# Optimization experiments

Hardware: AMD Instinct MI355X
Metric: run time of the kernel (lower is better)

The kernel has to match this reference:

```python
import jax, jax.numpy as jnp
import numpy as np

DIM = 768
HEADS = 12
HEAD_DIM = DIM // HEADS
HIDDEN = int(DIM * 4.0)
EPS = 1e-5


def _layernorm(x, g, b):
    mu = jnp.mean(x, axis=-1, keepdims=True)
    var = jnp.mean(jnp.square(x - mu), axis=-1, keepdims=True)
    return (x - mu) * jax.lax.rsqrt(var + EPS) * g + b


def setup_inputs() -> dict:
    key = jax.random.key(0)
    ks = jax.random.split(key, 8)
    s_in = 1.0 / np.sqrt(DIM)
    s_hid = 1.0 / np.sqrt(HIDDEN)
    return {
        "x": jax.random.normal(ks[0], (2, 2048, DIM), dtype=jnp.float32),
        "ln1_g": jnp.ones((DIM,), jnp.float32),
        "ln1_b": jnp.zeros((DIM,), jnp.float32),
        "w_qkv": jax.random.normal(ks[1], (DIM, 3 * DIM), jnp.float32) * s_in,
        "w_proj": jax.random.normal(ks[2], (DIM, DIM), jnp.float32) * s_in,
        "b_proj": jnp.zeros((DIM,), jnp.float32),
        "ln2_g": jnp.ones((DIM,), jnp.float32),
        "ln2_b": jnp.zeros((DIM,), jnp.float32),
        "w_fc1": jax.random.normal(ks[3], (DIM, HIDDEN), jnp.float32) * s_in,
        "b_fc1": jnp.zeros((HIDDEN,), jnp.float32),
        "w_fc2": jax.random.normal(ks[4], (HIDDEN, DIM), jnp.float32) * s_hid,
        "b_fc2": jnp.zeros((DIM,), jnp.float32),
    }


def reference(x, ln1_g, ln1_b, w_qkv, w_proj, b_proj, ln2_g, ln2_b, w_fc1, b_fc1, w_fc2, b_fc2):
    b, n, c = x.shape
    scale = HEAD_DIM ** -0.5

    # --- attention branch ---
    h = _layernorm(x, ln1_g, ln1_b)
    qkv = (h @ w_qkv).reshape(b, n, 3, HEADS, HEAD_DIM)
    q, k, v = jnp.moveaxis(qkv, 2, 0)          # each [b, n, H, hd]
    attn = jnp.einsum("bqhd,bkhd->bhqk", q, k) * scale
    attn = jax.nn.softmax(attn, axis=-1)       # [b, H, n, n] (naive, materialized)
    o = jnp.einsum("bhqk,bkhd->bqhd", attn, v).reshape(b, n, c)
    x = x + o @ w_proj + b_proj

    # --- MLP branch ---
    h2 = _layernorm(x, ln2_g, ln2_b)
    m = jax.nn.gelu(h2 @ w_fc1 + b_fc1, approximate=False)
    x = x + m @ w_fc2 + b_fc2
    return x
```

## Files before the change

kernel.cpp:

```cpp
#include <hip/hip_runtime.h>
#include <math.h>


typedef unsigned short u16;
typedef __attribute__((ext_vector_type(8))) short short8;
typedef __attribute__((ext_vector_type(4))) float f32x4;

#define TOKENS 4096
#define DIM    768
#define QKV_N  2304
#define HID    3072
#define NSEQ   2048
#define NHEAD  12
#define HDIM   64

__device__ __forceinline__ float bf2f(u16 u) {
  union { unsigned i; float f; } v; v.i = ((unsigned)u) << 16; return v.f;
}
__device__ __forceinline__ u16 f2bf(float f) {
  union { float f; unsigned i; } v; v.f = f;
  unsigned r = v.i + 0x7fffu + ((v.i >> 16) & 1u);
  return (u16)(r >> 16);
}
__device__ __forceinline__ unsigned cvt_pk_bf16(float lo, float hi) {
  unsigned r;
  asm("v_cvt_pk_bf16_f32 %0, %1, %2" : "=v"(r) : "v"(lo), "v"(hi));
  return r;
}
__device__ __forceinline__ void pl32swap(unsigned &a, unsigned &b) {
  asm("v_permlane32_swap_b32 %0, %1" : "+v"(a), "+v"(b));
}
__device__ __forceinline__ void pl16swap(unsigned &a, unsigned &b) {
  asm("v_permlane16_swap_b32 %0, %1" : "+v"(a), "+v"(b));
}

__device__ __forceinline__ void async_copy16(const u16* g, u16* l) {
  __builtin_amdgcn_global_load_lds(
      (const __attribute__((address_space(1))) unsigned int*)(unsigned long long)g,
      (__attribute__((address_space(3))) unsigned int*)(unsigned int)(unsigned long long)l,
      16, 0, 0);
}

__global__ __launch_bounds__(256) void prep_kernel(
    const float* __restrict__ x, const float* __restrict__ g,
    const float* __restrict__ b, u16* __restrict__ h,
    const float* __restrict__ in0, u16* __restrict__ out0,
    const float* __restrict__ in1, u16* __restrict__ out1,
    const float* __restrict__ in2, u16* __restrict__ out2,
    const float* __restrict__ in3, u16* __restrict__ out3) {
  const int tid = threadIdx.x;
  if (blockIdx.x < 1024) {
    int wave = tid >> 6, lane = tid & 63;
    int token = blockIdx.x * 4 + wave;
    float v[12];
    const float4* xr = (const float4*)(x + (size_t)token * DIM);
#pragma unroll
    for (int w = 0; w < 3; w++) {
      float4 q = xr[lane + w * 64];
      v[w * 4 + 0] = q.x; v[w * 4 + 1] = q.y; v[w * 4 + 2] = q.z; v[w * 4 + 3] = q.w;
    }
    float s = 0.f;
#pragma unroll
    for (int i = 0; i < 12; i++) s += v[i];
#pragma unroll
    for (int off = 32; off > 0; off >>= 1) s += __shfl_xor(s, off);
    float mu = s * (1.0f / DIM);
    float ss = 0.f;
#pragma unroll
    for (int i = 0; i < 12; i++) { float d = v[i] - mu; ss += d * d; }
#pragma unroll
    for (int off = 32; off > 0; off >>= 1) ss += __shfl_xor(ss, off);
    float rs = rsqrtf(ss * (1.0f / DIM) + 1e-5f);
    ushort4* orow = (ushort4*)(h + (size_t)token * DIM);
    const float4* g4 = (const float4*)g;
    const float4* b4 = (const float4*)b;
#pragma unroll
    for (int w = 0; w < 3; w++) {
      float4 gq = g4[lane + w * 64], bq = b4[lane + w * 64];
      ushort4 o;
      o.x = f2bf((v[w * 4 + 0] - mu) * rs * gq.x + bq.x);
      o.y = f2bf((v[w * 4 + 1] - mu) * rs * gq.y + bq.y);
      o.z = f2bf((v[w * 4 + 2] - mu) * rs * gq.z + bq.z);
      o.w = f2bf((v[w * 4 + 3] - mu) * rs * gq.w + bq.w);
      orow[lane + w * 64] = o;
    }
    return;
  }
  __shared__ u16 t[32][33];
  int bid = blockIdx.x - 1024, rem;
  const float* in; u16* out; int R, C;
  if (bid < 1728)      { in = in0; out = out0; R = 768;  C = 2304; rem = bid; }
  else if (bid < 2304) { in = in1; out = out1; R = 768;  C = 768;  rem = bid - 1728; }
  else if (bid < 4608) { in = in2; out = out2; R = 768;  C = 3072; rem = bid - 2304; }
  else                 { in = in3; out = out3; R = 3072; C = 768;  rem = bid - 4608; }
  int c0 = (rem % (C / 32)) * 32, r0 = (rem / (C / 32)) * 32;
  int tx = tid & 31, ty = tid >> 5;
#pragma unroll
  for (int i = 0; i < 4; i++)
    t[ty + i * 8][tx] = f2bf(in[(size_t)(r0 + ty + i * 8) * C + c0 + tx]);
  __syncthreads();
#pragma unroll
  for (int i = 0; i < 4; i++)
    out[(size_t)(c0 + ty + i * 8) * R + r0 + tx] = t[tx][ty + i * 8];
}

__global__ __launch_bounds__(256) void ln_kernel(const u16* __restrict__ xin,
                                                 const float* __restrict__ g,
                                                 const float* __restrict__ b,
                                                 u16* __restrict__ out) {
  int wave = threadIdx.x >> 6, lane = threadIdx.x & 63;
  int token = blockIdx.x * 4 + wave;
  float v[12];
  const ushort4* xr = (const ushort4*)(xin + (size_t)token * DIM);
#pragma unroll
  for (int w = 0; w < 3; w++) {
    ushort4 q = xr[lane + w * 64];
    v[w * 4 + 0] = bf2f(q.x); v[w * 4 + 1] = bf2f(q.y);
    v[w * 4 + 2] = bf2f(q.z); v[w * 4 + 3] = bf2f(q.w);
  }
  float s = 0.f;
#pragma unroll
  for (int i = 0; i < 12; i++) s += v[i];
#pragma unroll
  for (int off = 32; off > 0; off >>= 1) s += __shfl_xor(s, off);
  float mu = s * (1.0f / DIM);
  float ss = 0.f;
#pragma unroll
  for (int i = 0; i < 12; i++) { float d = v[i] - mu; ss += d * d; }
#pragma unroll
  for (int off = 32; off > 0; off >>= 1) ss += __shfl_xor(ss, off);
  float rs = rsqrtf(ss * (1.0f / DIM) + 1e-5f);

  ushort4* orow = (ushort4*)(out + (size_t)token * DIM);
  const float4* g4 = (const float4*)g;
  const float4* b4 = (const float4*)b;
#pragma unroll
  for (int w = 0; w < 3; w++) {
    float4 gq = g4[lane + w * 64], bq = b4[lane + w * 64];
    ushort4 o;
    o.x = f2bf((v[w * 4 + 0] - mu) * rs * gq.x + bq.x);
    o.y = f2bf((v[w * 4 + 1] - mu) * rs * gq.y + bq.y);
    o.z = f2bf((v[w * 4 + 2] - mu) * rs * gq.z + bq.z);
    o.w = f2bf((v[w * 4 + 3] - mu) * rs * gq.w + bq.w);
    orow[lane + w * 64] = o;
  }
}

template <int BM, int BN, int EPI, int NP>
__global__ __launch_bounds__(256, 3) void gemm_bt(
    const u16* __restrict__ A, const u16* __restrict__ BT,
    void* __restrict__ Cout, const float* __restrict__ bias,
    const void* __restrict__ resid, int M, int N, int K,
    u16* __restrict__ vtb) {
  constexpr int MT = BM / 32, NT = BN / 32;
  constexpr int ACH = BM / 16;
  constexpr int CPW = (BM + BN) / 64;
  __shared__ __align__(16) u16 Alds[NP][BM * 32];
  __shared__ __align__(16) u16 Blds[NP][BN * 32];
  const int tid = threadIdx.x;
  const int lane = tid & 63, wave = tid >> 6;
  const int wr = wave >> 1, wc = wave & 1;
  const int nby = M / BM;
  const int by = blockIdx.x % nby, bx = blockIdx.x / nby;
  const int bm = by * BM, bn = bx * BN;
  const int c16 = lane & 15, quad = lane >> 4;
  const int l4 = lane >> 2;
  const int lc = (((lane & 3) ^ ((l4 >> 1) & 3)) * 8);
  const int fsw = (c16 >> 1) & 3;

  f32x4 acc[MT][NT];
#pragma unroll
  for (int i = 0; i < MT; i++)
#pragma unroll
    for (int j = 0; j < NT; j++) acc[i][j] = (f32x4){0.f, 0.f, 0.f, 0.f};

  const u16* gsrc[CPW];
  u16* ldst[CPW];
  int hstep[CPW];
#pragma unroll
  for (int c = 0; c < CPW; c++) {
    int chunk = wave * CPW + c;
    if (chunk < ACH) {
      gsrc[c] = A + (size_t)(bm + chunk * 16 + l4) * K + lc;
      ldst[c] = Alds[0] + chunk * 512;
      hstep[c] = BM * 32;
    } else {
      int bc = chunk - ACH;
      gsrc[c] = BT + (size_t)(bn + bc * 16 + l4) * K + lc;
      ldst[c] = Blds[0] + bc * 512;
      hstep[c] = BN * 32;
    }
  }

  for (int kk = 0; kk < K; kk += 32 * NP) {
    __syncthreads();
#pragma unroll
    for (int c = 0; c < CPW; c++)
#pragma unroll
      for (int p = 0; p < NP; p++)
        async_copy16(gsrc[c] + kk + 32 * p, ldst[c] + p * hstep[c]);
    __syncthreads();
#pragma unroll
    for (int ks = 0; ks < NP; ks++) {
      short8 af[MT], bfr[NT];
#pragma unroll
      for (int mt = 0; mt < MT; mt++)
        af[mt] = *(const short8*)(Alds[ks] + (wr * (BM / 2) + mt * 16 + c16) * 32 +
                                  ((quad ^ fsw)) * 8);
#pragma unroll
      for (int nt = 0; nt < NT; nt++)
        bfr[nt] = *(const short8*)(Blds[ks] + (wc * (BN / 2) + nt * 16 + c16) * 32 +
                                   ((quad ^ fsw)) * 8);
#pragma unroll
      for (int mt = 0; mt < MT; mt++)
#pragma unroll
        for (int nt = 0; nt < NT; nt++)
          acc[mt][nt] = __builtin_amdgcn_mfma_f32_16x16x32_bf16(af[mt], bfr[nt],
                                                                acc[mt][nt], 0, 0, 0);
    }
  }

#pragma unroll
  for (int mt = 0; mt < MT; mt++) {
#pragma unroll
    for (int nt = 0; nt < NT; nt++) {
      int col = bn + wc * (BN / 2) + nt * 16 + c16;
      float bv = (EPI != 0) ? bias[col] : 0.f;
      int row0 = bm + wr * (BM / 2) + mt * 16 + quad * 4;
      if (EPI == 0 && col >= 2 * DIM) {
        int b = row0 >> 11;
        ushort4 pk;
        pk.x = f2bf(acc[mt][nt][0]); pk.y = f2bf(acc[mt][nt][1]);
        pk.z = f2bf(acc[mt][nt][2]); pk.w = f2bf(acc[mt][nt][3]);
        *(ushort4*)(vtb + ((size_t)b * DIM + col - 2 * DIM) * NSEQ + (row0 & 2047)) = pk;
        continue;
      }
#pragma unroll
      for (int r = 0; r < 4; r++) {
        int row = row0 + r;
        float vv = acc[mt][nt][r];
        if (EPI == 1) {
          vv += bv + ((const float*)resid)[(size_t)row * N + col];
          ((u16*)Cout)[(size_t)row * N + col] = f2bf(vv);
        } else if (EPI == 2) {
          vv += bv;
          vv = 0.5f * vv * (1.0f + erff(vv * 0.70710678118654752f));
          ((u16*)Cout)[(size_t)row * N + col] = f2bf(vv);
        } else if (EPI == 3) {
          vv += bv + bf2f(((const u16*)resid)[(size_t)row * N + col]);
          ((float*)Cout)[(size_t)row * N + col] = vv;
        } else {
          ((u16*)Cout)[(size_t)row * N + col] = f2bf(vv);
        }
      }
    }
  }
}

__global__ __launch_bounds__(256, 3) void attn_kernel(const u16* __restrict__ qkv,
                                                      const u16* __restrict__ vt,
                                                      u16* __restrict__ o) {
  const int tid = threadIdx.x;
  const int lane = tid & 63, wave = tid >> 6;
  const int c16 = lane & 15, quad = lane >> 4;
  const int wq = wave >> 1, wk = wave & 1;
  const int bh = blockIdx.x % (2 * NHEAD);
  const int qt = blockIdx.x / (2 * NHEAD);
  const int bb = bh / NHEAD, h = bh % NHEAD;
  __shared__ __align__(16) u16 Klds[2][64 * 64];
  __shared__ __align__(16) u16 Vtlds[2][64 * 64];
  const size_t base = (size_t)bb * NSEQ * QKV_N;
  const int q0 = qt * 64;
  const int sw = c16 & 7;

  short8 qf[2][2];
#pragma unroll
  for (int qs = 0; qs < 2; qs++) {
    const u16* qp = qkv + base + (size_t)(q0 + wq * 32 + qs * 16 + c16) * QKV_N + h * HDIM;
    qf[qs][0] = *(const short8*)(qp + quad * 8);
    qf[qs][1] = *(const short8*)(qp + 32 + quad * 8);
  }

  float Ls[2] = {0.f, 0.f};
  f32x4 Of[2][4];
#pragma unroll
  for (int qs = 0; qs < 2; qs++)
#pragma unroll
    for (int dt = 0; dt < 4; dt++) Of[qs][dt] = (f32x4){0.f, 0.f, 0.f, 0.f};

  const int srow = lane >> 3;
  const int schunk = (lane & 7) ^ srow;
  const int r0 = wave * 16;
  const u16* ksrc = qkv + base + (size_t)(r0 + srow) * QKV_N + DIM + h * HDIM + schunk * 8;
  const u16* vsrc = vt + ((size_t)bh * HDIM + r0 + srow) * NSEQ + schunk * 8;
  const float SC = 0.18033688011112042f;

#pragma unroll
  for (int j = 0; j < 2; j++) {
    async_copy16(ksrc + (size_t)(8 * j) * QKV_N, Klds[0] + r0 * 64 + 8 * j * 64);
    async_copy16(vsrc + (size_t)(8 * j) * NSEQ, Vtlds[0] + r0 * 64 + 8 * j * 64);
  }

  for (int it = 0; it < NSEQ / 64; it++) {
    const int cur = it & 1;
    __syncthreads();
    if (it + 1 < NSEQ / 64) {
      const int kt1 = (it + 1) * 64;
      u16* kd = Klds[cur ^ 1] + r0 * 64;
      u16* vd = Vtlds[cur ^ 1] + r0 * 64;
#pragma unroll
      for (int j = 0; j < 2; j++) {
        async_copy16(ksrc + (size_t)(kt1 + 8 * j) * QKV_N, kd + 8 * j * 64);
        async_copy16(vsrc + (size_t)(8 * j) * NSEQ + kt1, vd + 8 * j * 64);
      }
    }

    short8 kf0[2], kf1[2];
#pragma unroll
    for (int kt = 0; kt < 2; kt++) {
      const u16* krow = Klds[cur] + (wk * 32 + kt * 16 + c16) * 64;
      kf0[kt] = *(const short8*)(krow + (quad ^ sw) * 8);
      kf1[kt] = *(const short8*)(krow + ((quad + 4) ^ sw) * 8);
    }

    f32x4 St[2][2];
#pragma unroll
    for (int qs = 0; qs < 2; qs++)
#pragma unroll
      for (int kt = 0; kt < 2; kt++) {
        f32x4 s = (f32x4){0.f, 0.f, 0.f, 0.f};
        s = __builtin_amdgcn_mfma_f32_16x16x32_bf16(kf0[kt], qf[qs][0], s, 0, 0, 0);
        s = __builtin_amdgcn_mfma_f32_16x16x32_bf16(kf1[kt], qf[qs][1], s, 0, 0, 0);
        St[qs][kt] = s;
      }

    short8 vf[4];
#pragma unroll
    for (int dt = 0; dt < 4; dt++) {
      const u16* vrow = Vtlds[cur] + (dt * 16 + c16) * 64;
      vf[dt] = *(const short8*)(vrow + ((wk * 4 + quad) ^ sw) * 8);
    }

    short8 pf[2];
#pragma unroll
    for (int qs = 0; qs < 2; qs++) {
      float p[2][4];
#pragma unroll
      for (int kt = 0; kt < 2; kt++)
#pragma unroll
        for (int r = 0; r < 4; r++)
          p[kt][r] = __builtin_amdgcn_exp2f(St[qs][kt][r] * SC);
      Ls[qs] += ((p[0][0] + p[0][1]) + (p[0][2] + p[0][3])) +
                ((p[1][0] + p[1][1]) + (p[1][2] + p[1][3]));
      unsigned a0 = cvt_pk_bf16(p[0][0], p[0][1]);
      unsigned a1 = cvt_pk_bf16(p[0][2], p[0][3]);
      unsigned b0 = cvt_pk_bf16(p[1][0], p[1][1]);
      unsigned b1 = cvt_pk_bf16(p[1][2], p[1][3]);
      pl32swap(a0, b0);
      pl32swap(a1, b1);
      pl16swap(a0, b0);
      pl16swap(a1, b1);
      union { unsigned u[4]; short8 s; } pk_;
      pk_.u[0] = a0; pk_.u[1] = a1; pk_.u[2] = b0; pk_.u[3] = b1;
      pf[qs] = pk_.s;
    }

#pragma unroll
    for (int dt = 0; dt < 4; dt++)
#pragma unroll
      for (int qs = 0; qs < 2; qs++)
        Of[qs][dt] = __builtin_amdgcn_mfma_f32_16x16x32_bf16(pf[qs], vf[dt],
                                                             Of[qs][dt], 0, 0, 0);
  }

  __syncthreads();
  float* red = (float*)&Klds[0][0];
  float* lred = (float*)&Vtlds[0][0];
  if (wk == 1) {
    float* dst = red + wq * 2048;
#pragma unroll
    for (int qs = 0; qs < 2; qs++)
#pragma unroll
      for (int dt = 0; dt < 4; dt++)
        *(f32x4*)(dst + (qs * 4 + dt) * 256 + lane * 4) = Of[qs][dt];
    lred[wq * 128 + lane] = Ls[0];
    lred[wq * 128 + 64 + lane] = Ls[1];
  }
  __syncthreads();
  if (wk == 0) {
    const float* src = red + wq * 2048;
#pragma unroll
    for (int qs = 0; qs < 2; qs++)
#pragma unroll
      for (int dt = 0; dt < 4; dt++)
        Of[qs][dt] += *(const f32x4*)(src + (qs * 4 + dt) * 256 + lane * 4);
    float t0 = Ls[0] + lred[wq * 128 + lane];
    float t1 = Ls[1] + lred[wq * 128 + 64 + lane];
    t0 += __shfl_xor(t0, 16); t0 += __shfl_xor(t0, 32);
    t1 += __shfl_xor(t1, 16); t1 += __shfl_xor(t1, 32);
#pragma unroll
    for (int qs = 0; qs < 2; qs++) {
      float tq = qs ? t1 : t0;
#pragma unroll
      for (int r = 0; r < 4; r++) {
        float L = __shfl(tq, quad * 4 + r);
        int token = q0 + wq * 32 + qs * 16 + quad * 4 + r;
        u16* orow = o + (size_t)(bb * NSEQ + token) * DIM + h * HDIM;
#pragma unroll
        for (int dt = 0; dt < 4; dt++)
          orow[dt * 16 + c16] = f2bf(Of[qs][dt][r] / L);
      }
    }
  }
}

extern "C" void kernel_launch(void* const* d_in, const int* in_sizes, int n_in,
                              void* d_out, int out_size, void* d_ws, size_t ws_size,
                              hipStream_t stream) {
  (void)in_sizes; (void)n_in; (void)out_size; (void)ws_size;
  const float* x      = (const float*)d_in[0];
  const float* ln1_g  = (const float*)d_in[1];
  const float* ln1_b  = (const float*)d_in[2];
  const float* w_qkv  = (const float*)d_in[3];
  const float* w_proj = (const float*)d_in[4];
  const float* b_proj = (const float*)d_in[5];
  const float* ln2_g  = (const float*)d_in[6];
  const float* ln2_b  = (const float*)d_in[7];
  const float* w_fc1  = (const float*)d_in[8];
  const float* b_fc1  = (const float*)d_in[9];
  const float* w_fc2  = (const float*)d_in[10];
  const float* b_fc2  = (const float*)d_in[11];
  float* out = (float*)d_out;

  char* p = (char*)d_ws;
  u16* h_bf   = (u16*)p; p += (size_t)TOKENS * DIM * 2;
  u16* qkv_bf = (u16*)p; p += (size_t)TOKENS * QKV_N * 2;
  u16* o_bf   = (u16*)p; p += (size_t)TOKENS * DIM * 2;
  u16* x1_bf  = (u16*)p; p += (size_t)TOKENS * DIM * 2;
  u16* wprojT = (u16*)p; p += (size_t)DIM * DIM * 2;
  u16* wfc1T  = (u16*)p; p += (size_t)HID * DIM * 2;
  u16* wfc2T  = (u16*)p; p += (size_t)DIM * HID * 2;
  u16* wqkvT  = (u16*)p; p += (size_t)QKV_N * DIM * 2;
  u16* vtb    = (u16*)p; p += (size_t)TOKENS * DIM * 2;
  u16* m_bf   = qkv_bf;

  prep_kernel<<<dim3(1024 + 6912), 256, 0, stream>>>(
      x, ln1_g, ln1_b, h_bf,
      w_qkv, wqkvT, w_proj, wprojT, w_fc1, wfc1T, w_fc2, wfc2T);

  gemm_bt<64, 128, 0, 2><<<dim3((QKV_N / 128) * (TOKENS / 64)), 256, 0, stream>>>(
      h_bf, wqkvT, qkv_bf, nullptr, nullptr, TOKENS, QKV_N, DIM, vtb);
  attn_kernel<<<dim3(2 * NHEAD * (NSEQ / 64)), 256, 0, stream>>>(qkv_bf, vtb, o_bf);
  gemm_bt<64, 64, 1, 2><<<dim3((DIM / 64) * (TOKENS / 64)), 256, 0, stream>>>(
      o_bf, wprojT, x1_bf, b_proj, x, TOKENS, DIM, DIM, nullptr);
  ln_kernel<<<TOKENS / 4, 256, 0, stream>>>(x1_bf, ln2_g, ln2_b, h_bf);
  gemm_bt<64, 128, 2, 2><<<dim3((HID / 128) * (TOKENS / 64)), 256, 0, stream>>>(
      h_bf, wfc1T, m_bf, b_fc1, nullptr, TOKENS, HID, DIM, nullptr);
  gemm_bt<64, 64, 3, 4><<<dim3((DIM / 64) * (TOKENS / 64)), 256, 0, stream>>>(
      m_bf, wfc2T, out, b_fc2, x1_bf, TOKENS, DIM, HID, nullptr);
}
```

Baseline: 246.5 us.

## Double-buffer LDS tiles in projection and FC2 GEMMs to overlap loads with MFMA

Adds a DB template flag to the bf16 GEMM. When it is set, the kernel keeps two LDS buffers, prefetches the next K-slab into the alternate buffer, and runs MFMA on the current one, with one barrier per iteration instead of two. It is turned on for the output-projection and FC2 GEMMs, and FC2 drops from NP=4 to NP=2 so the LDS footprint stays bounded. The aim is to hide global-to-LDS latency, at the cost of more LDS per block, which could limit occupancy. Correctness depends on async_copy16 completing before the next barrier.

```diff
diff --git a/kernel.cpp b/kernel.cpp
--- a/kernel.cpp
+++ b/kernel.cpp
@@ -146,7 +146,7 @@
   }
 }
 
-template <int BM, int BN, int EPI, int NP>
+template <int BM, int BN, int EPI, int NP, int DB>
 __global__ __launch_bounds__(256, 3) void gemm_bt(
     const u16* __restrict__ A, const u16* __restrict__ BT,
     void* __restrict__ Cout, const float* __restrict__ bias,
@@ -155,8 +155,9 @@
   constexpr int MT = BM / 32, NT = BN / 32;
   constexpr int ACH = BM / 16;
   constexpr int CPW = (BM + BN) / 64;
-  __shared__ __align__(16) u16 Alds[NP][BM * 32];
-  __shared__ __align__(16) u16 Blds[NP][BN * 32];
+  constexpr int NB = DB ? 2 : 1;
+  __shared__ __align__(16) u16 Alds[NB][NP][BM * 32];
+  __shared__ __align__(16) u16 Blds[NB][NP][BN * 32];
   const int tid = threadIdx.x;
   const int lane = tid & 63, wave = tid >> 6;
   const int wr = wave >> 1, wc = wave & 1;
@@ -177,48 +178,74 @@
   const u16* gsrc[CPW];
   u16* ldst[CPW];
   int hstep[CPW];
+  int bstep[CPW];
 #pragma unroll
   for (int c = 0; c < CPW; c++) {
     int chunk = wave * CPW + c;
     if (chunk < ACH) {
       gsrc[c] = A + (size_t)(bm + chunk * 16 + l4) * K + lc;
-      ldst[c] = Alds[0] + chunk * 512;
+      ldst[c] = &Alds[0][0][0] + chunk * 512;
       hstep[c] = BM * 32;
+      bstep[c] = NP * BM * 32;
     } else {
       int bc = chunk - ACH;
       gsrc[c] = BT + (size_t)(bn + bc * 16 + l4) * K + lc;
-      ldst[c] = Blds[0] + bc * 512;
+      ldst[c] = &Blds[0][0][0] + bc * 512;
       hstep[c] = BN * 32;
-    }
-  }
-
-  for (int kk = 0; kk < K; kk += 32 * NP) {
-    __syncthreads();
-#pragma unroll
-    for (int c = 0; c < CPW; c++)
-#pragma unroll
-      for (int p = 0; p < NP; p++)
-        async_copy16(gsrc[c] + kk + 32 * p, ldst[c] + p * hstep[c]);
-    __syncthreads();
-#pragma unroll
-    for (int ks = 0; ks < NP; ks++) {
-      short8 af[MT], bfr[NT];
-#pragma unroll
-      for (int mt = 0; mt < MT; mt++)
-        af[mt] = *(const short8*)(Alds[ks] + (wr * (BM / 2) + mt * 16 + c16) * 32 +
-                                  ((quad ^ fsw)) * 8);
-#pragma unroll
-      for (int nt = 0; nt < NT; nt++)
-        bfr[nt] = *(const short8*)(Blds[ks] + (wc * (BN / 2) + nt * 16 + c16) * 32 +
-                                   ((quad ^ fsw)) * 8);
-#pragma unroll
-      for (int mt = 0; mt < MT; mt++)
-#pragma unroll
-        for (int nt = 0; nt < NT; nt++)
-          acc[mt][nt] = __builtin_amdgcn_mfma_f32_16x16x32_bf16(af[mt], bfr[nt],
-                                                                acc[mt][nt], 0, 0, 0);
-    }
-  }
+      bstep[c] = NP * BN * 32;
+    }
+  }
+
+#define GB_STAGE(KK, BUF)                                                   \
+  {                                                                         \
+    _Pragma("unroll")                                                       \
+    for (int c = 0; c < CPW; c++)                                           \
+      _Pragma("unroll")                                                     \
+      for (int p = 0; p < NP; p++)                                          \
+        async_copy16(gsrc[c] + (KK) + 32 * p,                               \
+                     ldst[c] + (BUF) * bstep[c] + p * hstep[c]);            \
+  }
+#define GB_COMPUTE(BUF)                                                     \
+  {                                                                         \
+    _Pragma("unroll")                                                       \
+    for (int ks = 0; ks < NP; ks++) {                                       \
+      short8 af[MT], bfr[NT];                                               \
+      _Pragma("unroll")                                                     \
+      for (int mt = 0; mt < MT; mt++)                                       \
+        af[mt] = *(const short8*)(&Alds[BUF][ks][0] +                       \
+                  (wr * (BM / 2) + mt * 16 + c16) * 32 + ((quad ^ fsw)) * 8); \
+      _Pragma("unroll")                                                     \
+      for (int nt = 0; nt < NT; nt++)                                       \
+        bfr[nt] = *(const short8*)(&Blds[BUF][ks][0] +                      \
+                  (wc * (BN / 2) + nt * 16 + c16) * 32 + ((quad ^ fsw)) * 8); \
+      _Pragma("unroll")                                                     \
+      for (int mt = 0; mt < MT; mt++)                                       \
+        _Pragma("unroll")                                                   \
+        for (int nt = 0; nt < NT; nt++)                                     \
+          acc[mt][nt] = __builtin_amdgcn_mfma_f32_16x16x32_bf16(            \
+              af[mt], bfr[nt], acc[mt][nt], 0, 0, 0);                       \
+    }                                                                       \
+  }
+
+  if constexpr (DB == 0) {
+    for (int kk = 0; kk < K; kk += 32 * NP) {
+      __syncthreads();
+      GB_STAGE(kk, 0);
+      __syncthreads();
+      GB_COMPUTE(0);
+    }
+  } else {
+    GB_STAGE(0, 0);
+    const int nr = K / (32 * NP);
+    for (int r = 0; r < nr; r++) {
+      const int cb = r & 1;
+      __syncthreads();
+      if (r + 1 < nr) GB_STAGE((r + 1) * 32 * NP, cb ^ 1);
+      GB_COMPUTE(cb);
+    }
+  }
+#undef GB_STAGE
+#undef GB_COMPUTE
 
 #pragma unroll
   for (int mt = 0; mt < MT; mt++) {
@@ -448,14 +475,14 @@
       x, ln1_g, ln1_b, h_bf,
       w_qkv, wqkvT, w_proj, wprojT, w_fc1, wfc1T, w_fc2, wfc2T);
 
-  gemm_bt<64, 128, 0, 2><<<dim3((QKV_N / 128) * (TOKENS / 64)), 256, 0, stream>>>(
+  gemm_bt<64, 128, 0, 2, 0><<<dim3((QKV_N / 128) * (TOKENS / 64)), 256, 0, stream>>>(
       h_bf, wqkvT, qkv_bf, nullptr, nullptr, TOKENS, QKV_N, DIM, vtb);
   attn_kernel<<<dim3(2 * NHEAD * (NSEQ / 64)), 256, 0, stream>>>(qkv_bf, vtb, o_bf);
-  gemm_bt<64, 64, 1, 2><<<dim3((DIM / 64) * (TOKENS / 64)), 256, 0, stream>>>(
+  gemm_bt<64, 64, 1, 2, 1><<<dim3((DIM / 64) * (TOKENS / 64)), 256, 0, stream>>>(
       o_bf, wprojT, x1_bf, b_proj, x, TOKENS, DIM, DIM, nullptr);
   ln_kernel<<<TOKENS / 4, 256, 0, stream>>>(x1_bf, ln2_g, ln2_b, h_bf);
-  gemm_bt<64, 128, 2, 2><<<dim3((HID / 128) * (TOKENS / 64)), 256, 0, stream>>>(
+  gemm_bt<64, 128, 2, 2, 0><<<dim3((HID / 128) * (TOKENS / 64)), 256, 0, stream>>>(
       h_bf, wfc1T, m_bf, b_fc1, nullptr, TOKENS, HID, DIM, nullptr);
-  gemm_bt<64, 64, 3, 4><<<dim3((DIM / 64) * (TOKENS / 64)), 256, 0, stream>>>(
+  gemm_bt<64, 64, 3, 2, 1><<<dim3((DIM / 64) * (TOKENS / 64)), 256, 0, stream>>>(
       m_bf, wfc2T, out, b_fc2, x1_bf, TOKENS, DIM, HID, nullptr);
 }
```

Measured after the change: 240.4 us, median of 2. -2.5%, faster.
